# Kernel tuning notes

Hardware: AMD Instinct MI355X
Metric: run time of the kernel (lower is better)

The kernel has to match this reference:

```python
import jax, jax.numpy as jnp
import numpy as np


def setup_inputs() -> dict:
    key = jax.random.key(0)
    k1, k2, k3 = jax.random.split(key, 3)
    B, Cin, Cout, K, H, W = 32, 128, 128, 4, 112, 112
    x = jax.random.normal(k1, (B, Cin, H, W), dtype=jnp.float32)
    # Conv2d 1x1 weights: [K, out_ch, in_ch] (kernel dims of size 1 squeezed)
    expert_w = jax.random.normal(k2, (K, Cout, Cin), dtype=jnp.float32) * (1.0 / np.sqrt(Cin))
    gate_w = jax.random.normal(k3, (K, Cin), dtype=jnp.float32) * (1.0 / np.sqrt(Cin))
    gate_b = jnp.zeros((K,), dtype=jnp.float32)
    return {"x": x, "expert_w": expert_w, "gate_w": gate_w, "gate_b": gate_b}


def reference(x, expert_w, gate_w, gate_b):
    # Gate: global average pool -> 1x1 conv -> softmax over K
    pooled = jnp.mean(x, axis=(2, 3))                      # [B, Cin]
    logits = pooled @ gate_w.T + gate_b                    # [B, K]
    g = jax.nn.softmax(logits, axis=1)                     # [B, K]
    # Combine expert weights per sample (math-equivalent to sum_k g_k * conv_k(x))
    w_b = jnp.einsum('bk,koi->boi', g, expert_w)           # [B, Cout, Cin]
    out = jnp.einsum('boi,bihw->bohw', w_b, x)             # [B, Cout, H, W]
    return out
```

## Files before the change

### kernel.cpp

```cpp
#include <hip/hip_runtime.h>
#include <hip/hip_bf16.h>
#include <stdint.h>

#define B_     32
#define CIN    128
#define COUT   128
#define KEXP   4
#define HW_    12544
#define NCHUNK 196

typedef __attribute__((ext_vector_type(8))) short bf16x8;
typedef __attribute__((ext_vector_type(4))) float f32x4;

static __device__ __forceinline__ ushort f2bf(float f) {
    uint32_t u = __builtin_bit_cast(uint32_t, f);
    u += 0x7FFFu + ((u >> 16) & 1u);
    return (ushort)(u >> 16);
}


__global__ __launch_bounds__(256) void prep_kernel(const float* __restrict__ x,
                                                   short* __restrict__ xbf,
                                                   float* __restrict__ partial) {
    const int b  = blockIdx.y;
    const int cx = blockIdx.x;
    const int p0 = cx * 64;
    const int t  = threadIdx.x;
    const int pg  = t & 15;
    const int cg8 = t >> 4;

    const float* __restrict__ xr = x + (size_t)b * CIN * HW_
                                 + (size_t)(cg8 * 8) * HW_ + p0 + pg * 4;
    f32x4 va[8];
    #pragma unroll
    for (int i = 0; i < 8; ++i)
        va[i] = __builtin_nontemporal_load((const f32x4*)(xr + (size_t)i * HW_));

    float ps[8];
    #pragma unroll
    for (int i = 0; i < 8; ++i) ps[i] = (va[i][0] + va[i][1]) + (va[i][2] + va[i][3]);
    #pragma unroll
    for (int m = 1; m < 16; m <<= 1) {
        #pragma unroll
        for (int i = 0; i < 8; ++i) ps[i] += __shfl_xor(ps[i], m, 64);
    }
    if (pg == 0) {
        float* pdst = partial + ((size_t)b * NCHUNK + cx) * CIN + cg8 * 8;
        f32x4 v0 = {ps[0], ps[1], ps[2], ps[3]};
        f32x4 v1 = {ps[4], ps[5], ps[6], ps[7]};
        *(f32x4*)pdst = v0;
        *(f32x4*)(pdst + 4) = v1;
    }

    short* __restrict__ xd = xbf + (size_t)b * HW_ * CIN + (size_t)p0 * CIN + cg8 * 8;
    #pragma unroll
    for (int j = 0; j < 4; ++j) {
        bf16x8 pk;
        #pragma unroll
        for (int i = 0; i < 8; ++i) pk[i] = (short)f2bf(va[i][j]);
        *(bf16x8*)(xd + (size_t)(pg * 4 + j) * CIN) = pk;
    }
}

__global__ __launch_bounds__(256) void gate2_kernel(const float* __restrict__ partial,
                                                    const float* __restrict__ gate_w,
                                                    const float* __restrict__ gate_b,
                                                    const float* __restrict__ expert_w,
                                                    short* __restrict__ wmix) {
    const int b = blockIdx.x;
    const int t = threadIdx.x;
    __shared__ float pl[CIN];
    if (t < CIN) {
        float s = 0.f;
        const float* pp = partial + (size_t)b * NCHUNK * CIN + t;
        for (int c = 0; c < NCHUNK; ++c) s += pp[(size_t)c * CIN];
        pl[t] = s * (1.0f / HW_);
    }
    __syncthreads();

    const int wid = t >> 6, lane = t & 63;
    __shared__ float logits[KEXP];
    __shared__ float gsh[KEXP];
    {
        float s = pl[lane] * gate_w[wid * CIN + lane]
                + pl[64 + lane] * gate_w[wid * CIN + 64 + lane];
        #pragma unroll
        for (int off = 32; off > 0; off >>= 1) s += __shfl_down(s, off, 64);
        if (lane == 0) logits[wid] = s + gate_b[wid];
    }
    __syncthreads();
    if (t == 0) {
        float m = fmaxf(fmaxf(logits[0], logits[1]), fmaxf(logits[2], logits[3]));
        float e0 = expf(logits[0] - m), e1 = expf(logits[1] - m);
        float e2 = expf(logits[2] - m), e3 = expf(logits[3] - m);
        float inv = 1.f / (e0 + e1 + e2 + e3);
        gsh[0] = e0 * inv; gsh[1] = e1 * inv; gsh[2] = e2 * inv; gsh[3] = e3 * inv;
    }
    __syncthreads();
    const float g0 = gsh[0], g1 = gsh[1], g2 = gsh[2], g3 = gsh[3];
    for (int idx = t; idx < COUT * CIN; idx += 256) {
        float w = g0 * expert_w[idx]
                + g1 * expert_w[COUT * CIN + idx]
                + g2 * expert_w[2 * COUT * CIN + idx]
                + g3 * expert_w[3 * COUT * CIN + idx];
        wmix[b * COUT * CIN + idx] = (short)f2bf(w);
    }
}

__global__ __launch_bounds__(256, 4) void conv2_kernel(const short* __restrict__ xbf,
                                                       const short* __restrict__ wmix,
                                                       float* __restrict__ out) {
    __shared__ char wlds[COUT * 256];
    const int b   = blockIdx.y;
    const int t   = threadIdx.x;
    const int px0 = blockIdx.x * 128;

    {
        const uint4* __restrict__ wsrc = (const uint4*)(wmix + (size_t)b * COUT * CIN);
        #pragma unroll
        for (int pass = 0; pass < 8; ++pass) {
            int o  = (t >> 4) + pass * 16;
            int i4 = t & 15;
            uint4 v = wsrc[o * 16 + i4];
            *(uint4*)(wlds + o * 256 + ((i4 ^ (o & 15)) << 4)) = v;
        }
    }

    const int wave = t >> 6;
    const int lane = t & 63;
    const int n = lane & 15;
    const int h = lane >> 4;

    const short* __restrict__ xb = xbf + (size_t)b * HW_ * CIN
                                 + (size_t)(px0 + wave * 16 + n) * CIN + h * 8;

    bf16x8 xa[4], xc[4];
    #pragma unroll
    for (int kk = 0; kk < 4; ++kk) xa[kk] = *(const bf16x8*)(xb + kk * 32);
    #pragma unroll
    for (int kk = 0; kk < 4; ++kk) xc[kk] = *(const bf16x8*)(xb + 64 * CIN + kk * 32);

    __syncthreads();

    f32x4 acc[8];

    #pragma unroll
    for (int ot = 0; ot < 8; ++ot) acc[ot] = (f32x4){0.f, 0.f, 0.f, 0.f};
    #pragma unroll
    for (int ot = 0; ot < 8; ++ot) {
        const int o = ot * 16 + n;
        #pragma unroll
        for (int kk = 0; kk < 4; ++kk) {
            bf16x8 wfrag = *(const bf16x8*)(wlds + o * 256 + (((kk * 4 + h) ^ n) << 4));
            acc[ot] = __builtin_amdgcn_mfma_f32_16x16x32_bf16(xa[kk], wfrag, acc[ot], 0, 0, 0);
        }
    }
    {
        float* __restrict__ ob = out + (size_t)b * COUT * HW_ + px0 + wave * 16 + h * 4;
        #pragma unroll
        for (int ot = 0; ot < 8; ++ot)
            __builtin_nontemporal_store(acc[ot], (f32x4*)(ob + (size_t)(ot * 16 + n) * HW_));
    }

    #pragma unroll
    for (int ot = 0; ot < 8; ++ot) acc[ot] = (f32x4){0.f, 0.f, 0.f, 0.f};
    #pragma unroll
    for (int ot = 0; ot < 8; ++ot) {
        const int o = ot * 16 + n;
        #pragma unroll
        for (int kk = 0; kk < 4; ++kk) {
            bf16x8 wfrag = *(const bf16x8*)(wlds + o * 256 + (((kk * 4 + h) ^ n) << 4));
            acc[ot] = __builtin_amdgcn_mfma_f32_16x16x32_bf16(xc[kk], wfrag, acc[ot], 0, 0, 0);
        }
    }
    {
        float* __restrict__ ob = out + (size_t)b * COUT * HW_ + px0 + 64 + wave * 16 + h * 4;
        #pragma unroll
        for (int ot = 0; ot < 8; ++ot)
            __builtin_nontemporal_store(acc[ot], (f32x4*)(ob + (size_t)(ot * 16 + n) * HW_));
    }
}


__global__ __launch_bounds__(256) void pool_kernel(const float* __restrict__ x,
                                                   float* __restrict__ pooled) {
    const int row = blockIdx.x;
    const float4* __restrict__ x4 = (const float4*)(x + (size_t)row * HW_);
    const int t = threadIdx.x;
    float s = 0.f;
    for (int idx = t; idx < HW_ / 4; idx += 256) {
        float4 v = x4[idx];
        s += (v.x + v.y) + (v.z + v.w);
    }
    #pragma unroll
    for (int off = 32; off > 0; off >>= 1) s += __shfl_down(s, off, 64);
    __shared__ float wsum[4];
    if ((t & 63) == 0) wsum[t >> 6] = s;
    __syncthreads();
    if (t == 0) pooled[row] = (wsum[0] + wsum[1] + wsum[2] + wsum[3]) * (1.0f / HW_);
}

__global__ __launch_bounds__(256) void gate_kernel(const float* __restrict__ pooled,
                                                   const float* __restrict__ gate_w,
                                                   const float* __restrict__ gate_b,
                                                   const float* __restrict__ expert_w,
                                                   short* __restrict__ wmix) {
    const int b = blockIdx.x;
    const int t = threadIdx.x;
    const int wid = t >> 6, lane = t & 63;
    __shared__ float logits[KEXP];
    __shared__ float gsh[KEXP];
    {
        float p0 = pooled[b * CIN + lane];
        float p1 = pooled[b * CIN + 64 + lane];
        float s = p0 * gate_w[wid * CIN + lane] + p1 * gate_w[wid * CIN + 64 + lane];
        #pragma unroll
        for (int off = 32; off > 0; off >>= 1) s += __shfl_down(s, off, 64);
        if (lane == 0) logits[wid] = s + gate_b[wid];
    }
    __syncthreads();
    if (t == 0) {
        float m = fmaxf(fmaxf(logits[0], logits[1]), fmaxf(logits[2], logits[3]));
        float e0 = expf(logits[0] - m), e1 = expf(logits[1] - m);
        float e2 = expf(logits[2] - m), e3 = expf(logits[3] - m);
        float inv = 1.f / (e0 + e1 + e2 + e3);
        gsh[0] = e0 * inv; gsh[1] = e1 * inv; gsh[2] = e2 * inv; gsh[3] = e3 * inv;
    }
    __syncthreads();
    const float g0 = gsh[0], g1 = gsh[1], g2 = gsh[2], g3 = gsh[3];
    for (int idx = t; idx < COUT * CIN; idx += 256) {
        float w = g0 * expert_w[idx]
                + g1 * expert_w[COUT * CIN + idx]
                + g2 * expert_w[2 * COUT * CIN + idx]
                + g3 * expert_w[3 * COUT * CIN + idx];
        wmix[b * COUT * CIN + idx] = (short)f2bf(w);
    }
}

__global__ __launch_bounds__(256, 4) void conv_fb_kernel(const float* __restrict__ x,
                                                         const short* __restrict__ wmix,
                                                         float* __restrict__ out) {
    __shared__ char wlds[COUT * 256];
    __shared__ char xlds[64 * 256];
    const int b  = blockIdx.y;
    const int p0 = blockIdx.x * 64;
    const int t  = threadIdx.x;

    {
        const uint4* __restrict__ wsrc = (const uint4*)(wmix + (size_t)b * COUT * CIN);
        #pragma unroll
        for (int pass = 0; pass < 8; ++pass) {
            int o  = (t >> 4) + pass * 16;
            int i4 = t & 15;
            uint4 v = wsrc[o * 16 + i4];
            *(uint4*)(wlds + o * 256 + ((i4 ^ (o & 15)) << 4)) = v;
        }
    }
    {
        const int pg = t & 15;
        const int cg = t >> 4;
        #pragma unroll
        for (int p = 0; p < 2; ++p) {
            const int cin0 = p * 64 + cg * 4;
            const float* xrow = x + (size_t)b * CIN * HW_ + (size_t)cin0 * HW_ + p0 + pg * 4;
            float va[4][4];
            #pragma unroll
            for (int i = 0; i < 4; ++i) {
                float4 v = *(const float4*)(xrow + (size_t)i * HW_);
                va[i][0] = v.x; va[i][1] = v.y; va[i][2] = v.z; va[i][3] = v.w;
            }
            #pragma unroll
            for (int j = 0; j < 4; ++j) {
                const int pix = pg * 4 + j;
                uint32_t lo = (uint32_t)f2bf(va[0][j]) | ((uint32_t)f2bf(va[1][j]) << 16);
                uint32_t hi = (uint32_t)f2bf(va[2][j]) | ((uint32_t)f2bf(va[3][j]) << 16);
                int byte = (pix * 256 + cin0 * 2) ^ ((pix & 7) << 4);
                uint2 w2; w2.x = lo; w2.y = hi;
                *(uint2*)(xlds + byte) = w2;
            }
        }
    }

    const int wave = t >> 6;
    const int lane = t & 63;
    const int n = lane & 15;
    const int h = lane >> 4;

    __syncthreads();

    bf16x8 xfrag[4];
    {
        const int pixl = wave * 16 + n;
        #pragma unroll
        for (int kk = 0; kk < 4; ++kk) {
            int byte = (pixl * 256 + kk * 64 + h * 16) ^ ((pixl & 7) << 4);
            xfrag[kk] = *(const bf16x8*)(xlds + byte);
        }
    }

    f32x4 acc[8];
    #pragma unroll
    for (int ot = 0; ot < 8; ++ot) acc[ot] = (f32x4){0.f, 0.f, 0.f, 0.f};

    #pragma unroll
    for (int ot = 0; ot < 8; ++ot) {
        const int o = ot * 16 + n;
        #pragma unroll
        for (int kk = 0; kk < 4; ++kk) {
            bf16x8 wfrag = *(const bf16x8*)(wlds + o * 256 + (((kk * 4 + h) ^ n) << 4));
            acc[ot] = __builtin_amdgcn_mfma_f32_16x16x32_bf16(xfrag[kk], wfrag, acc[ot], 0, 0, 0);
        }
    }

    float* __restrict__ ob = out + (size_t)b * COUT * HW_ + p0 + wave * 16 + h * 4;
    #pragma unroll
    for (int ot = 0; ot < 8; ++ot)
        __builtin_nontemporal_store(acc[ot], (f32x4*)(ob + (size_t)(ot * 16 + n) * HW_));
}

extern "C" void kernel_launch(void* const* d_in, const int* in_sizes, int n_in,
                              void* d_out, int out_size, void* d_ws, size_t ws_size,
                              hipStream_t stream) {
    const float* x        = (const float*)d_in[0];
    const float* expert_w = (const float*)d_in[1];
    const float* gate_w   = (const float*)d_in[2];
    const float* gate_b   = (const float*)d_in[3];
    float* out = (float*)d_out;

    const size_t PARTIAL_B = (size_t)B_ * NCHUNK * CIN * 4;
    const size_t WMIX_B    = (size_t)B_ * COUT * CIN * 2;
    const size_t XBF_B     = (size_t)B_ * HW_ * CIN * 2;
    const size_t NEED      = PARTIAL_B + WMIX_B + XBF_B;

    if (ws_size >= NEED) {
        float* partial = (float*)d_ws;
        short* wmix    = (short*)((char*)d_ws + PARTIAL_B);
        short* xbf     = (short*)((char*)d_ws + PARTIAL_B + WMIX_B);

        prep_kernel<<<dim3(NCHUNK, B_), 256, 0, stream>>>(x, xbf, partial);
        gate2_kernel<<<dim3(B_), 256, 0, stream>>>(partial, gate_w, gate_b, expert_w, wmix);
        conv2_kernel<<<dim3(HW_ / 128, B_), 256, 0, stream>>>(xbf, wmix, out);
    } else {
        float* pooled = (float*)d_ws;
        short* wmix   = (short*)((char*)d_ws + 16384);
        pool_kernel<<<dim3(B_ * CIN), 256, 0, stream>>>(x, pooled);
        gate_kernel<<<dim3(B_), 256, 0, stream>>>(pooled, gate_w, gate_b, expert_w, wmix);
        conv_fb_kernel<<<dim3(HW_ / 64, B_), 256, 0, stream>>>(x, wmix, out);
    }
}
```

Before: 142.1 us.

## Pre-swizzle x and mixed weights into MFMA fragment layout, use 32x32x16 MFMA

The prep and gate kernels now write the bf16 activations and the mixed weights directly in per-lane MFMA fragment order. The conv kernel can then load each fragment with one contiguous 16-byte access per lane, and the weight copy into LDS becomes a plain copy with no XOR swizzle. The conv also switches from 16x16x32 to 32x32x16 bf16 MFMA, so each wave handles 32 pixels across four 32-row output tiles. In exchange, output stores become scalar per-element nontemporal stores (32 contiguous floats per row across lanes) instead of f32x4 vectors, which may raise store instruction count.

```diff
diff --git a/kernel.cpp b/kernel.cpp
--- a/kernel.cpp
+++ b/kernel.cpp
@@ -8,9 +8,11 @@
 #define KEXP   4
 #define HW_    12544
 #define NCHUNK 196
+#define NPT    392
 
 typedef __attribute__((ext_vector_type(8))) short bf16x8;
 typedef __attribute__((ext_vector_type(4))) float f32x4;
+typedef __attribute__((ext_vector_type(16))) float f32x16;
 
 static __device__ __forceinline__ ushort f2bf(float f) {
     uint32_t u = __builtin_bit_cast(uint32_t, f);
@@ -20,7 +22,7 @@
 
 
 __global__ __launch_bounds__(256) void prep_kernel(const float* __restrict__ x,
-                                                   short* __restrict__ xbf,
+                                                   short* __restrict__ xbf2,
                                                    float* __restrict__ partial) {
     const int b  = blockIdx.y;
     const int cx = blockIdx.x;
@@ -52,13 +54,15 @@
         *(f32x4*)(pdst + 4) = v1;
     }
 
-    short* __restrict__ xd = xbf + (size_t)b * HW_ * CIN + (size_t)p0 * CIN + cg8 * 8;
-    #pragma unroll
-    for (int j = 0; j < 4; ++j) {
+    short* __restrict__ xd = xbf2
+        + ((size_t)(b * NPT + cx * 2 + (pg >> 3)) * 8 + (cg8 >> 1)) * 512
+        + ((cg8 & 1) * 32 + (pg & 7) * 4) * 8;
+    #pragma unroll
+    for (int jj = 0; jj < 4; ++jj) {
         bf16x8 pk;
         #pragma unroll
-        for (int i = 0; i < 8; ++i) pk[i] = (short)f2bf(va[i][j]);
-        *(bf16x8*)(xd + (size_t)(pg * 4 + j) * CIN) = pk;
+        for (int i = 0; i < 8; ++i) pk[i] = (short)f2bf(va[i][jj]);
+        *(bf16x8*)(xd + jj * 8) = pk;
     }
 }
 
@@ -66,7 +70,7 @@
                                                     const float* __restrict__ gate_w,
                                                     const float* __restrict__ gate_b,
                                                     const float* __restrict__ expert_w,
-                                                    short* __restrict__ wmix) {
+                                                    short* __restrict__ wmix2) {
     const int b = blockIdx.x;
     const int t = threadIdx.x;
     __shared__ float pl[CIN];
@@ -103,81 +107,62 @@
                 + g1 * expert_w[COUT * CIN + idx]
                 + g2 * expert_w[2 * COUT * CIN + idx]
                 + g3 * expert_w[3 * COUT * CIN + idx];
-        wmix[b * COUT * CIN + idx] = (short)f2bf(w);
-    }
-}
-
-__global__ __launch_bounds__(256, 4) void conv2_kernel(const short* __restrict__ xbf,
-                                                       const short* __restrict__ wmix,
+        const int o = idx >> 7, c = idx & 127;
+        const int dst = ((b * 4 + (o >> 5)) * 8 + (c >> 4)) * 512
+                      + (((c >> 3) & 1) * 32 + (o & 31)) * 8 + (c & 7);
+        wmix2[dst] = (short)f2bf(w);
+    }
+}
+
+__global__ __launch_bounds__(256, 4) void conv3_kernel(const short* __restrict__ xbf2,
+                                                       const short* __restrict__ wmix2,
                                                        float* __restrict__ out) {
-    __shared__ char wlds[COUT * 256];
-    const int b   = blockIdx.y;
-    const int t   = threadIdx.x;
-    const int px0 = blockIdx.x * 128;
-
-    {
-        const uint4* __restrict__ wsrc = (const uint4*)(wmix + (size_t)b * COUT * CIN);
+    __shared__ short wlds[4 * 8 * 512];
+    const int b = blockIdx.y;
+    const int t = threadIdx.x;
+
+    {
+        const short* __restrict__ wsrc = wmix2 + (size_t)b * 16384;
         #pragma unroll
         for (int pass = 0; pass < 8; ++pass) {
-            int o  = (t >> 4) + pass * 16;
-            int i4 = t & 15;
-            uint4 v = wsrc[o * 16 + i4];
-            *(uint4*)(wlds + o * 256 + ((i4 ^ (o & 15)) << 4)) = v;
+            uint4 v = *(const uint4*)(wsrc + pass * 2048 + t * 8);
+            *(uint4*)(wlds + pass * 2048 + t * 8) = v;
         }
     }
 
     const int wave = t >> 6;
     const int lane = t & 63;
-    const int n = lane & 15;
-    const int h = lane >> 4;
-
-    const short* __restrict__ xb = xbf + (size_t)b * HW_ * CIN
-                                 + (size_t)(px0 + wave * 16 + n) * CIN + h * 8;
-
-    bf16x8 xa[4], xc[4];
-    #pragma unroll
-    for (int kk = 0; kk < 4; ++kk) xa[kk] = *(const bf16x8*)(xb + kk * 32);
-    #pragma unroll
-    for (int kk = 0; kk < 4; ++kk) xc[kk] = *(const bf16x8*)(xb + 64 * CIN + kk * 32);
-
-    __syncthreads();
-
-    f32x4 acc[8];
-
-    #pragma unroll
-    for (int ot = 0; ot < 8; ++ot) acc[ot] = (f32x4){0.f, 0.f, 0.f, 0.f};
-    #pragma unroll
-    for (int ot = 0; ot < 8; ++ot) {
-        const int o = ot * 16 + n;
-        #pragma unroll
-        for (int kk = 0; kk < 4; ++kk) {
-            bf16x8 wfrag = *(const bf16x8*)(wlds + o * 256 + (((kk * 4 + h) ^ n) << 4));
-            acc[ot] = __builtin_amdgcn_mfma_f32_16x16x32_bf16(xa[kk], wfrag, acc[ot], 0, 0, 0);
-        }
-    }
-    {
-        float* __restrict__ ob = out + (size_t)b * COUT * HW_ + px0 + wave * 16 + h * 4;
-        #pragma unroll
-        for (int ot = 0; ot < 8; ++ot)
-            __builtin_nontemporal_store(acc[ot], (f32x4*)(ob + (size_t)(ot * 16 + n) * HW_));
-    }
-
-    #pragma unroll
-    for (int ot = 0; ot < 8; ++ot) acc[ot] = (f32x4){0.f, 0.f, 0.f, 0.f};
-    #pragma unroll
-    for (int ot = 0; ot < 8; ++ot) {
-        const int o = ot * 16 + n;
-        #pragma unroll
-        for (int kk = 0; kk < 4; ++kk) {
-            bf16x8 wfrag = *(const bf16x8*)(wlds + o * 256 + (((kk * 4 + h) ^ n) << 4));
-            acc[ot] = __builtin_amdgcn_mfma_f32_16x16x32_bf16(xc[kk], wfrag, acc[ot], 0, 0, 0);
-        }
-    }
-    {
-        float* __restrict__ ob = out + (size_t)b * COUT * HW_ + px0 + 64 + wave * 16 + h * 4;
-        #pragma unroll
-        for (int ot = 0; ot < 8; ++ot)
-            __builtin_nontemporal_store(acc[ot], (f32x4*)(ob + (size_t)(ot * 16 + n) * HW_));
+    const int pt   = blockIdx.x * 4 + wave;
+
+    const short* __restrict__ xb = xbf2 + ((size_t)(b * NPT + pt) * 8) * 512 + lane * 8;
+    bf16x8 bfrag[8];
+    #pragma unroll
+    for (int f = 0; f < 8; ++f)
+        bfrag[f] = *(const bf16x8*)(xb + f * 512);
+
+    __syncthreads();
+
+    const int rowadd = 4 * (lane >> 5);
+    float* __restrict__ ob = out + (size_t)b * COUT * HW_ + pt * 32 + (lane & 31);
+
+    #pragma unroll
+    for (int ct = 0; ct < 4; ++ct) {
+        f32x16 acc;
+        #pragma unroll
+        for (int r = 0; r < 16; ++r) acc[r] = 0.f;
+
+        const short* __restrict__ wl = wlds + (ct * 8) * 512 + lane * 8;
+        #pragma unroll
+        for (int f = 0; f < 8; ++f) {
+            bf16x8 afrag = *(const bf16x8*)(wl + f * 512);
+            acc = __builtin_amdgcn_mfma_f32_32x32x16_bf16(afrag, bfrag[f], acc, 0, 0, 0);
+        }
+
+        #pragma unroll
+        for (int r = 0; r < 16; ++r) {
+            const int cout = ct * 32 + (r & 3) + 8 * (r >> 2) + rowadd;
+            __builtin_nontemporal_store(acc[r], ob + (size_t)cout * HW_);
+        }
     }
 }
 
@@ -334,12 +319,12 @@
 
     if (ws_size >= NEED) {
         float* partial = (float*)d_ws;
-        short* wmix    = (short*)((char*)d_ws + PARTIAL_B);
-        short* xbf     = (short*)((char*)d_ws + PARTIAL_B + WMIX_B);
-
-        prep_kernel<<<dim3(NCHUNK, B_), 256, 0, stream>>>(x, xbf, partial);
-        gate2_kernel<<<dim3(B_), 256, 0, stream>>>(partial, gate_w, gate_b, expert_w, wmix);
-        conv2_kernel<<<dim3(HW_ / 128, B_), 256, 0, stream>>>(xbf, wmix, out);
+        short* wmix2   = (short*)((char*)d_ws + PARTIAL_B);
+        short* xbf2    = (short*)((char*)d_ws + PARTIAL_B + WMIX_B);
+
+        prep_kernel<<<dim3(NCHUNK, B_), 256, 0, stream>>>(x, xbf2, partial);
+        gate2_kernel<<<dim3(B_), 256, 0, stream>>>(partial, gate_w, gate_b, expert_w, wmix2);
+        conv3_kernel<<<dim3(NPT / 4, B_), 256, 0, stream>>>(xbf2, wmix2, out);
     } else {
         float* pooled = (float*)d_ws;
         short* wmix   = (short*)((char*)d_ws + 16384);
```

New measurement: 130.3 us. 1.09x faster.
